# Kernel tuning notes

Hardware: AMD Instinct MI355X
Metric: run time of the kernel (lower is better)

## Reference

```python
import jax, jax.numpy as jnp
import numpy as np


def setup_inputs() -> dict:
    key = jax.random.key(0)
    k1, k2 = jax.random.split(key)
    B, N, M, D = 4, 8192, 8192, 3
    input1 = jax.random.normal(k1, (B, N, D), dtype=jnp.float32)
    input2 = jax.random.normal(k2, (B, M, D), dtype=jnp.float32)
    return {"input1": input1, "input2": input2}


def reference(input1, input2):
    x2 = jnp.sum(input1 * input1, axis=-1)              # [B, N]
    y2 = jnp.sum(input2 * input2, axis=-1)              # [B, M]
    xy = jnp.einsum('bnd,bmd->bnm', input1, input2)     # [B, N, M]
    d2 = x2[:, :, None] + y2[:, None, :] - 2.0 * xy     # [B, N, M]
    d2 = jnp.maximum(d2, 0.0)
    dist1 = jnp.min(d2, axis=2)  # [B, N] nearest in input2 for each point in input1
    dist2 = jnp.min(d2, axis=1)  # [B, M] nearest in input1 for each point in input2
    # Chamfer loss: mean of both directional terms
    return jnp.mean(dist1) + jnp.mean(dist2)
```

## Files before the change

### kernel.cpp

```cpp
#include <hip/hip_runtime.h>

#define NB    4
#define NPTS  8192
#define QPL   2
#define QPB   (64 * QPL)
#define WPB   8
#define UNR   8

typedef float v2f __attribute__((ext_vector_type(2)));

struct TPair { v2f xx, yy, zz, ww; };

__global__ void pack_pts(const float* __restrict__ a, const float* __restrict__ b,
                         float4* __restrict__ q4a, float4* __restrict__ q4b,
                         TPair* __restrict__ tpa, TPair* __restrict__ tpb) {
    const int npair = NB * NPTS / 2;
    int i = blockIdx.x * blockDim.x + threadIdx.x;
    const float* src = a;
    float4* q4 = q4a;  TPair* tp = tpa;
    int p = i;
    if (i >= npair) { src = b; q4 = q4b; tp = tpb; p = i - npair; }

    float x0 = src[6*p+0], y0 = src[6*p+1], z0 = src[6*p+2];
    float x1 = src[6*p+3], y1 = src[6*p+4], z1 = src[6*p+5];
    float w0 = 0.5f * (x0*x0 + y0*y0 + z0*z0);
    float w1 = 0.5f * (x1*x1 + y1*y1 + z1*z1);
    q4[2*p]   = make_float4(x0, y0, z0, w0);
    q4[2*p+1] = make_float4(x1, y1, z1, w1);
    TPair t;
    t.xx = (v2f){x0, x1}; t.yy = (v2f){y0, y1};
    t.zz = (v2f){z0, z1}; t.ww = (v2f){w0, w1};
    tp[p] = t;
}

#define GROUP(NQX, NQY, NQZ, XX, YY, ZZ, WW, ACC) do {                         \
    v2f r_;                                                                    \
    asm("v_pk_mul_f32 %0, %1, %2"     : "=v"(r_) : "v"(NQX), "s"(XX));         \
    asm("v_pk_fma_f32 %0, %1, %2, %0" : "+v"(r_) : "v"(NQY), "s"(YY));         \
    asm("v_pk_fma_f32 %0, %1, %2, %0" : "+v"(r_) : "v"(NQZ), "s"(ZZ));         \
    asm("v_pk_add_f32 %0, %0, %1"     : "+v"(r_) : "s"(WW));                   \
    asm("v_min3_f32 %0, %0, %1, %2"   : "+v"(ACC) : "v"(r_.x), "v"(r_.y));     \
} while (0)

__launch_bounds__(512)
__global__ void chamfer_min(const float4* __restrict__ q4a, const float4* __restrict__ q4b,
                            const TPair* __restrict__ tpa, const TPair* __restrict__ tpb,
                            float* __restrict__ accum) {
    __shared__ float red[QPL][WPB][64];

    const int dir = blockIdx.y;
    const int bb  = blockIdx.x / (NPTS / QPB);
    const int blk = blockIdx.x % (NPTS / QPB);

    const float4* __restrict__ Q = (dir == 0 ? q4a : q4b) + bb * NPTS;
    const TPair*  __restrict__ T = (dir == 0 ? tpb : tpa) + bb * (NPTS / 2);

    const int lane = threadIdx.x & 63;
    const int wave = __builtin_amdgcn_readfirstlane((int)(threadIdx.x >> 6));

    const float4 qa = Q[blk * QPB + lane];
    const float4 qb = Q[blk * QPB + 64 + lane];
    v2f nax = (v2f){-qa.x, -qa.x}, nay = (v2f){-qa.y, -qa.y}, naz = (v2f){-qa.z, -qa.z};
    v2f nbx = (v2f){-qb.x, -qb.x}, nby = (v2f){-qb.y, -qb.y}, nbz = (v2f){-qb.z, -qb.z};

    const int PPW = NPTS / 2 / WPB;
    const TPair* __restrict__ Tw = T + wave * PPW;

    float aA0 = 1e30f, aA1 = 1e30f, aA2 = 1e30f, aA3 = 1e30f;
    float aB0 = 1e30f, aB1 = 1e30f, aB2 = 1e30f, aB3 = 1e30f;

#pragma unroll 1
    for (int p = 0; p < PPW; p += UNR) {
        TPair t0 = Tw[p + 0], t1 = Tw[p + 1], t2 = Tw[p + 2], t3 = Tw[p + 3];
        TPair t4 = Tw[p + 4], t5 = Tw[p + 5], t6 = Tw[p + 6], t7 = Tw[p + 7];
        GROUP(nax, nay, naz, t0.xx, t0.yy, t0.zz, t0.ww, aA0);
        GROUP(nbx, nby, nbz, t0.xx, t0.yy, t0.zz, t0.ww, aB0);
        GROUP(nax, nay, naz, t1.xx, t1.yy, t1.zz, t1.ww, aA1);
        GROUP(nbx, nby, nbz, t1.xx, t1.yy, t1.zz, t1.ww, aB1);
        GROUP(nax, nay, naz, t2.xx, t2.yy, t2.zz, t2.ww, aA2);
        GROUP(nbx, nby, nbz, t2.xx, t2.yy, t2.zz, t2.ww, aB2);
        GROUP(nax, nay, naz, t3.xx, t3.yy, t3.zz, t3.ww, aA3);
        GROUP(nbx, nby, nbz, t3.xx, t3.yy, t3.zz, t3.ww, aB3);
        GROUP(nax, nay, naz, t4.xx, t4.yy, t4.zz, t4.ww, aA0);
        GROUP(nbx, nby, nbz, t4.xx, t4.yy, t4.zz, t4.ww, aB0);
        GROUP(nax, nay, naz, t5.xx, t5.yy, t5.zz, t5.ww, aA1);
        GROUP(nbx, nby, nbz, t5.xx, t5.yy, t5.zz, t5.ww, aB1);
        GROUP(nax, nay, naz, t6.xx, t6.yy, t6.zz, t6.ww, aA2);
        GROUP(nbx, nby, nbz, t6.xx, t6.yy, t6.zz, t6.ww, aB2);
        GROUP(nax, nay, naz, t7.xx, t7.yy, t7.zz, t7.ww, aA3);
        GROUP(nbx, nby, nbz, t7.xx, t7.yy, t7.zz, t7.ww, aB3);
    }
    float accA = fminf(fminf(aA0, aA1), fminf(aA2, aA3));
    float accB = fminf(fminf(aB0, aB1), fminf(aB2, aB3));

    red[0][wave][lane] = accA;
    red[1][wave][lane] = accB;
    __syncthreads();

    if (threadIdx.x < 128) {
        const int q = threadIdx.x >> 6;
        float v = red[q][0][lane];
#pragma unroll
        for (int w = 1; w < WPB; ++w) v = fminf(v, red[q][w][lane]);
        const float qw = (q == 0) ? qa.w : qb.w;
        float dist = fmaxf(2.0f * (qw + v), 0.0f);
        for (int off = 32; off > 0; off >>= 1)
            dist += __shfl_xor(dist, off, 64);
        if (lane == 0) atomicAdd(&accum[dir], dist);
    }
}

__global__ void finish(const float* __restrict__ accum, float* __restrict__ out) {
    out[0] = (accum[0] + accum[1]) * (1.0f / (NB * NPTS));
}

extern "C" void kernel_launch(void* const* d_in, const int* in_sizes, int n_in,
                              void* d_out, int out_size, void* d_ws, size_t ws_size,
                              hipStream_t stream) {
    const float* in1 = (const float*)d_in[0];
    const float* in2 = (const float*)d_in[1];

    const int tot   = NB * NPTS;
    const int npair = tot / 2;

    char* ws = (char*)d_ws;
    float*  accum = (float*)ws;
    float4* q4a   = (float4*)(ws + 256);
    float4* q4b   = q4a + tot;
    TPair*  tpa   = (TPair*)(q4b + tot);
    TPair*  tpb   = tpa + npair;

    hipMemsetAsync(accum, 0, 2 * sizeof(float), stream);

    pack_pts<<<dim3((2 * npair) / 256), 256, 0, stream>>>(in1, in2, q4a, q4b, tpa, tpb);

    dim3 grid(NB * (NPTS / QPB), 2);
    chamfer_min<<<grid, 512, 0, stream>>>(q4a, q4b, tpa, tpb, accum);

    finish<<<1, 1, 0, stream>>>(accum, (float*)d_out);
}
```

Baseline: 71.10 us.

## Load target pairs via global vector loads into VGPRs with 16 waves per block

Target point pairs were previously read as wave-uniform values into scalar registers. They are now fetched with inline-asm global_load_dwordx4 into vector registers and used as VGPR operands of the packed math. Waves per block double from 8 to 16, so each wave walks half as many pairs, with a smaller unroll and fewer partial-min accumulators. This trades scalar-cache loads for redundant per-lane vector loads, and it waits on vmcnt(0) each iteration, which removes overlap between loads and compute.

After: 132.8 us. 1.87x slower.

```diff
diff --git a/kernel.cpp b/kernel.cpp
--- a/kernel.cpp
+++ b/kernel.cpp
@@ -4,10 +4,11 @@
 #define NPTS  8192
 #define QPL   2
 #define QPB   (64 * QPL)
-#define WPB   8
-#define UNR   8
+#define WPB   16
+#define UNR   4
 
 typedef float v2f __attribute__((ext_vector_type(2)));
+typedef float v4f __attribute__((ext_vector_type(4)));
 
 struct TPair { v2f xx, yy, zz, ww; };
 
@@ -33,16 +34,24 @@
     tp[p] = t;
 }
 
-#define GROUP(NQX, NQY, NQZ, XX, YY, ZZ, WW, ACC) do {                         \
+#define GLD(DST, OFF) \
+    asm volatile("global_load_dwordx4 %0, %1, %2 offset:" OFF \
+                 : "=v"(DST) : "v"(voff), "s"(Tb))
+
+#define GROUPV(NQX, NQY, NQZ, TL, TH, ACC) do {                                \
+    v2f xx_ = __builtin_shufflevector(TL, TL, 0, 1);                           \
+    v2f yy_ = __builtin_shufflevector(TL, TL, 2, 3);                           \
+    v2f zz_ = __builtin_shufflevector(TH, TH, 0, 1);                           \
+    v2f ww_ = __builtin_shufflevector(TH, TH, 2, 3);                           \
     v2f r_;                                                                    \
-    asm("v_pk_mul_f32 %0, %1, %2"     : "=v"(r_) : "v"(NQX), "s"(XX));         \
-    asm("v_pk_fma_f32 %0, %1, %2, %0" : "+v"(r_) : "v"(NQY), "s"(YY));         \
-    asm("v_pk_fma_f32 %0, %1, %2, %0" : "+v"(r_) : "v"(NQZ), "s"(ZZ));         \
-    asm("v_pk_add_f32 %0, %0, %1"     : "+v"(r_) : "s"(WW));                   \
+    asm volatile("v_pk_mul_f32 %0, %1, %2" : "=v"(r_) : "v"(NQX), "v"(xx_));   \
+    asm("v_pk_fma_f32 %0, %1, %2, %0" : "+v"(r_) : "v"(NQY), "v"(yy_));        \
+    asm("v_pk_fma_f32 %0, %1, %2, %0" : "+v"(r_) : "v"(NQZ), "v"(zz_));        \
+    asm("v_pk_add_f32 %0, %0, %1"     : "+v"(r_) : "v"(ww_));                  \
     asm("v_min3_f32 %0, %0, %1, %2"   : "+v"(ACC) : "v"(r_.x), "v"(r_.y));     \
 } while (0)
 
-__launch_bounds__(512)
+__launch_bounds__(1024, 8)
 __global__ void chamfer_min(const float4* __restrict__ q4a, const float4* __restrict__ q4b,
                             const TPair* __restrict__ tpa, const TPair* __restrict__ tpb,
                             float* __restrict__ accum) {
@@ -64,34 +73,32 @@
     v2f nbx = (v2f){-qb.x, -qb.x}, nby = (v2f){-qb.y, -qb.y}, nbz = (v2f){-qb.z, -qb.z};
 
     const int PPW = NPTS / 2 / WPB;
-    const TPair* __restrict__ Tw = T + wave * PPW;
+    const TPair* __restrict__ Tb = T;
+    unsigned voff = (unsigned)(wave * PPW * sizeof(TPair));
 
-    float aA0 = 1e30f, aA1 = 1e30f, aA2 = 1e30f, aA3 = 1e30f;
-    float aB0 = 1e30f, aB1 = 1e30f, aB2 = 1e30f, aB3 = 1e30f;
+    float aA0 = 1e30f, aA1 = 1e30f, aB0 = 1e30f, aB1 = 1e30f;
 
 #pragma unroll 1
-    for (int p = 0; p < PPW; p += UNR) {
-        TPair t0 = Tw[p + 0], t1 = Tw[p + 1], t2 = Tw[p + 2], t3 = Tw[p + 3];
-        TPair t4 = Tw[p + 4], t5 = Tw[p + 5], t6 = Tw[p + 6], t7 = Tw[p + 7];
-        GROUP(nax, nay, naz, t0.xx, t0.yy, t0.zz, t0.ww, aA0);
-        GROUP(nbx, nby, nbz, t0.xx, t0.yy, t0.zz, t0.ww, aB0);
-        GROUP(nax, nay, naz, t1.xx, t1.yy, t1.zz, t1.ww, aA1);
-        GROUP(nbx, nby, nbz, t1.xx, t1.yy, t1.zz, t1.ww, aB1);
-        GROUP(nax, nay, naz, t2.xx, t2.yy, t2.zz, t2.ww, aA2);
-        GROUP(nbx, nby, nbz, t2.xx, t2.yy, t2.zz, t2.ww, aB2);
-        GROUP(nax, nay, naz, t3.xx, t3.yy, t3.zz, t3.ww, aA3);
-        GROUP(nbx, nby, nbz, t3.xx, t3.yy, t3.zz, t3.ww, aB3);
-        GROUP(nax, nay, naz, t4.xx, t4.yy, t4.zz, t4.ww, aA0);
-        GROUP(nbx, nby, nbz, t4.xx, t4.yy, t4.zz, t4.ww, aB0);
-        GROUP(nax, nay, naz, t5.xx, t5.yy, t5.zz, t5.ww, aA1);
-        GROUP(nbx, nby, nbz, t5.xx, t5.yy, t5.zz, t5.ww, aB1);
-        GROUP(nax, nay, naz, t6.xx, t6.yy, t6.zz, t6.ww, aA2);
-        GROUP(nbx, nby, nbz, t6.xx, t6.yy, t6.zz, t6.ww, aB2);
-        GROUP(nax, nay, naz, t7.xx, t7.yy, t7.zz, t7.ww, aA3);
-        GROUP(nbx, nby, nbz, t7.xx, t7.yy, t7.zz, t7.ww, aB3);
+    for (int it = 0; it < PPW / UNR; ++it) {
+        v4f t0l, t0h, t1l, t1h, t2l, t2h, t3l, t3h;
+        GLD(t0l, "0");  GLD(t0h, "16");
+        GLD(t1l, "32"); GLD(t1h, "48");
+        GLD(t2l, "64"); GLD(t2h, "80");
+        GLD(t3l, "96"); GLD(t3h, "112");
+        asm volatile("s_waitcnt vmcnt(0)");
+        __builtin_amdgcn_sched_barrier(0);
+        GROUPV(nax, nay, naz, t0l, t0h, aA0);
+        GROUPV(nbx, nby, nbz, t0l, t0h, aB0);
+        GROUPV(nax, nay, naz, t1l, t1h, aA1);
+        GROUPV(nbx, nby, nbz, t1l, t1h, aB1);
+        GROUPV(nax, nay, naz, t2l, t2h, aA0);
+        GROUPV(nbx, nby, nbz, t2l, t2h, aB0);
+        GROUPV(nax, nay, naz, t3l, t3h, aA1);
+        GROUPV(nbx, nby, nbz, t3l, t3h, aB1);
+        voff += UNR * sizeof(TPair);
     }
-    float accA = fminf(fminf(aA0, aA1), fminf(aA2, aA3));
-    float accB = fminf(fminf(aB0, aB1), fminf(aB2, aB3));
+    float accA = fminf(aA0, aA1);
+    float accB = fminf(aB0, aB1);
 
     red[0][wave][lane] = accA;
     red[1][wave][lane] = accB;
@@ -135,7 +142,7 @@
     pack_pts<<<dim3((2 * npair) / 256), 256, 0, stream>>>(in1, in2, q4a, q4b, tpa, tpb);
 
     dim3 grid(NB * (NPTS / QPB), 2);
-    chamfer_min<<<grid, 512, 0, stream>>>(q4a, q4b, tpa, tpb, accum);
+    chamfer_min<<<grid, 1024, 0, stream>>>(q4a, q4b, tpa, tpb, accum);
 
     finish<<<1, 1, 0, stream>>>(accum, (float*)d_out);
 }
```
